# Kernel optimization log

Measured on AMD Instinct MI355X. Metric: run time of the kernel, lower is better.

## Reference

```python
import jax, jax.numpy as jnp
import numpy as np

B, C, N = 8, 128, 32768


def setup_inputs() -> dict:
    key = jax.random.key(0)
    ks = jax.random.split(key, 16)
    def g(k, shape, scale=0.05):
        return jax.random.normal(k, shape, dtype=jnp.float32) * scale
    return {
        "x": jax.random.normal(ks[0], (B, C, N), dtype=jnp.float32),
        "y": jax.random.normal(ks[1], (B, C, N), dtype=jnp.float32),
        "q_w": g(ks[2], (C, C)), "q_b": g(ks[3], (C,)),
        "k_w": g(ks[4], (C, C)), "k_b": g(ks[5], (C,)),
        "v1_w": g(ks[6], (C, C)), "v1_b": g(ks[7], (C,)),
        "v2_w": g(ks[8], (C, C)), "v2_b": g(ks[9], (C,)),
        "t1_w": g(ks[10], (2 * C, 2 * C)), "t1_b": g(ks[11], (2 * C,)),
        "t2_w": g(ks[12], (C, 2 * C)), "t2_b": g(ks[13], (C,)),
    }


def reference(x, y, q_w, q_b, k_w, k_b, v1_w, v1_b, v2_w, v2_b,
              t1_w, t1_b, t2_w, t2_b):
    # num_heads = 1, head_dim = C. Conv1d with kernel 1 == pointwise matmul.
    c = x.shape[1]
    pconv = lambda w, b, z: jnp.einsum('oc,bcn->bon', w, z) + b[None, :, None]
    x_q = pconv(q_w, q_b, y)    # [B,C,N]
    x_k = pconv(k_w, k_b, x)    # [B,C,N]
    x_v = pconv(v1_w, v1_b, x)  # [B,C,N]
    y_v = pconv(v2_w, v2_b, y)  # [B,C,N]
    x_con = jnp.concatenate([x_q, x_k], axis=1)                 # [B,2C,N]
    v_con = jnp.concatenate([y_v.transpose(0, 2, 1),
                             x_v.transpose(0, 2, 1)], axis=2)   # [B,N,2C]
    scale = jnp.sqrt(jnp.float32(2 * c))
    energy = jnp.einsum('bcn,bdn->bcd', x_con, x_con) / scale   # [B,2C,2C]
    e = jax.nn.relu(energy @ t1_w.T + t1_b)                     # [B,2C,2C]
    e = jax.nn.relu(e @ t2_w.T + t2_b)                          # [B,2C,C]
    attn = jax.nn.softmax(e, axis=-1)                           # [B,2C,C]
    x_r = jnp.einsum('bnd,bdc->bnc', v_con, attn)               # [B,N,C]
    return x_r.transpose(0, 2, 1)                               # [B,C,N]
```

## Files before the change

### kernel.cpp

```cpp
#include <hip/hip_runtime.h>

constexpr int CH   = 128;
constexpr int TWOC = 256;
constexpr int NPTS = 32768;
constexpr int NB   = 8;
constexpr int KC   = 2048;

constexpr int KC3    = 1024;
constexpr int KSTAGE = 128;
constexpr int NST    = KC3 / KSTAGE;
constexpr int NCHUNK = NPTS / KC3;

typedef _Float16 half8 __attribute__((ext_vector_type(8)));
typedef float floatx4 __attribute__((ext_vector_type(4)));

constexpr size_t OFF_G  = 0;
constexpr size_t OFF_S  = 524288;
constexpr size_t OFF_P  = 526336;
constexpr size_t OFF_H  = 528384;
constexpr size_t OFF_E  = 1052672;
constexpr size_t OFF_E1 = 1576960;
constexpr size_t OFF_E2 = 2101248;
constexpr size_t OFF_AT = 2363392;
constexpr size_t OFF_C0 = 2625536;
constexpr size_t OFF_MH = 2626560;
constexpr size_t OFF_ZH = 2757632;
constexpr size_t OFF_GP = OFF_ZH + 33554432;
constexpr size_t GP_LEN = (size_t)3 * NB * NCHUNK * 128 * 128;
constexpr size_t WS_NEED_NEW = (OFF_ZH + 33554432) * sizeof(float);
constexpr size_t WS_NEED_V3  = (OFF_GP + GP_LEN) * sizeof(float);


__global__ __launch_bounds__(256) void convert_kernel(
    const float* __restrict__ x, const float* __restrict__ y,
    _Float16* __restrict__ Zh, float* __restrict__ S)
{
  const int seg = blockIdx.x;
  const int r   = blockIdx.y;
  const int b   = blockIdx.z;
  const float* src = ((r < CH) ? (y + ((size_t)b*CH + r)*NPTS)
                               : (x + ((size_t)b*CH + (r-CH))*NPTS)) + (size_t)seg*4096;
  _Float16* dst = Zh + ((size_t)b*TWOC + r)*NPTS + (size_t)seg*4096;
  const int tid = threadIdx.x;

  float s = 0.f;
  const float4* s4 = (const float4*)(src + tid*16);
  union { uint4 u; _Float16 h[8]; } p0, p1;
  float4 a = s4[0], bq = s4[1], c = s4[2], d = s4[3];
  p0.h[0]=(_Float16)a.x;  p0.h[1]=(_Float16)a.y;  p0.h[2]=(_Float16)a.z;  p0.h[3]=(_Float16)a.w;
  p0.h[4]=(_Float16)bq.x; p0.h[5]=(_Float16)bq.y; p0.h[6]=(_Float16)bq.z; p0.h[7]=(_Float16)bq.w;
  p1.h[0]=(_Float16)c.x;  p1.h[1]=(_Float16)c.y;  p1.h[2]=(_Float16)c.z;  p1.h[3]=(_Float16)c.w;
  p1.h[4]=(_Float16)d.x;  p1.h[5]=(_Float16)d.y;  p1.h[6]=(_Float16)d.z;  p1.h[7]=(_Float16)d.w;
  s += a.x+a.y+a.z+a.w + bq.x+bq.y+bq.z+bq.w + c.x+c.y+c.z+c.w + d.x+d.y+d.z+d.w;
  *(uint4*)(dst + tid*16)     = p0.u;
  *(uint4*)(dst + tid*16 + 8) = p1.u;

  for (int off = 32; off > 0; off >>= 1) s += __shfl_down(s, off);
  if ((tid & 63) == 0) atomicAdd(&S[b*TWOC + r], s);
}

__global__ __launch_bounds__(256) void gram_mfma3(
    const _Float16* __restrict__ Zh, float* __restrict__ G, float* __restrict__ GP)
{
  __shared__ __align__(16) _Float16 As[2][128 * KSTAGE];
  __shared__ __align__(16) _Float16 Bs[2][128 * KSTAGE];

  const int hw    = blockIdx.x;
  const int xcd   = hw & 7;
  const int local = hw >> 3;
  const int t     = local % 3;
  const int grp   = local / 3;
  const int gidx  = xcd * 32 + grp;
  const int kc    = gidx & 31;
  const int b     = gidx >> 5;

  const int i0 = (t == 0) ? 0 : CH;
  const int j0 = (t == 2) ? CH : 0;
  const _Float16* Ar = Zh + ((size_t)b*TWOC + i0)*NPTS + (size_t)kc*KC3;
  const _Float16* Br = Zh + ((size_t)b*TWOC + j0)*NPTS + (size_t)kc*KC3;

  const int tid   = threadIdx.x;
  const int lane  = tid & 63;
  const int wave  = tid >> 6;
  const int mbase = (wave & 1) * 64;
  const int nbase = (wave >> 1) * 64;
  const int m0    = lane & 15;
  const int quad  = lane >> 4;

  const int srow = (wave * 512) >> 4;

#define STAGE(buf, k0)                                                        \
  {                                                                           \
    _Pragma("unroll")                                                         \
    for (int i = 0; i < 8; i++) {                                             \
      const int s = wave*512 + i*64 + lane;                                   \
      const int r = s >> 4;                                                   \
      const int g = s & 15;                                                   \
      const int gs = g ^ (r & 7);                                             \
      __builtin_amdgcn_global_load_lds(                                       \
        (const __attribute__((address_space(1))) void*)(Ar + (size_t)r*NPTS + (k0) + gs*8), \
        (__attribute__((address_space(3))) void*)&As[buf][(wave*512 + i*64)*8], \
        16, 0, 0);                                                            \
      __builtin_amdgcn_global_load_lds(                                       \
        (const __attribute__((address_space(1))) void*)(Br + (size_t)r*NPTS + (k0) + gs*8), \
        (__attribute__((address_space(3))) void*)&Bs[buf][(wave*512 + i*64)*8], \
        16, 0, 0);                                                            \
    }                                                                         \
  }

  floatx4 acc[4][4];
  #pragma unroll
  for (int i = 0; i < 4; i++)
    #pragma unroll
    for (int j = 0; j < 4; j++) acc[i][j] = (floatx4){0.f,0.f,0.f,0.f};

  (void)srow;
  STAGE(0, 0);

  int cur = 0;
  for (int st = 0; st < NST; ++st) {
    if (st + 1 < NST) {
      STAGE(cur ^ 1, (st + 1) * KSTAGE);
      asm volatile("s_waitcnt vmcnt(16)" ::: "memory");
    } else {
      asm volatile("s_waitcnt vmcnt(0)" ::: "memory");
    }
    __builtin_amdgcn_s_barrier();

    #pragma unroll
    for (int kk = 0; kk < 4; kk++) {
      half8 af[4], bf[4];
      #pragma unroll
      for (int i = 0; i < 4; i++) {
        const int ra = mbase + i*16 + m0;
        const int ga = (kk*4 + quad) ^ (ra & 7);
        af[i] = *(const half8*)&As[cur][ra*KSTAGE + ga*8];
        const int rb = nbase + i*16 + m0;
        const int gb = (kk*4 + quad) ^ (rb & 7);
        bf[i] = *(const half8*)&Bs[cur][rb*KSTAGE + gb*8];
      }
      #pragma unroll
      for (int i = 0; i < 4; i++)
        #pragma unroll
        for (int j = 0; j < 4; j++)
          acc[i][j] = __builtin_amdgcn_mfma_f32_16x16x32_f16(af[i], bf[j], acc[i][j], 0, 0, 0);
    }

    __builtin_amdgcn_s_barrier();
    cur ^= 1;
  }
#undef STAGE

  if (GP != nullptr) {
    float* gp = GP + (((size_t)(b*3 + t)*NCHUNK + kc) * (128*128));
    #pragma unroll
    for (int i = 0; i < 4; i++)
      #pragma unroll
      for (int j = 0; j < 4; j++)
        #pragma unroll
        for (int rg = 0; rg < 4; rg++) {
          const int row = mbase + i*16 + quad*4 + rg;
          const int col = nbase + j*16 + m0;
          gp[row*128 + col] = acc[i][j][rg];
        }
  } else {
    #pragma unroll
    for (int i = 0; i < 4; i++)
      #pragma unroll
      for (int j = 0; j < 4; j++)
        #pragma unroll
        for (int rg = 0; rg < 4; rg++) {
          const int row = i0 + mbase + i*16 + quad*4 + rg;
          const int col = j0 + nbase + j*16 + m0;
          atomicAdd(&G[((size_t)b*TWOC + row)*TWOC + col], acc[i][j][rg]);
        }
  }
}

__global__ __launch_bounds__(256) void greduce_kernel(
    const float* __restrict__ GP, float* __restrict__ G)
{
  const int t   = blockIdx.y;
  const int b   = blockIdx.z;
  const int idx = blockIdx.x * 256 + threadIdx.x;
  const float* gp = GP + ((size_t)(b*3 + t)*NCHUNK) * (128*128) + idx;
  float s = 0.f;
  #pragma unroll
  for (int k = 0; k < NCHUNK; k++) s += gp[(size_t)k * (128*128)];
  const int i0 = (t == 0) ? 0 : CH;
  const int j0 = (t == 2) ? CH : 0;
  const int row = idx >> 7, col = idx & 127;
  G[((size_t)b*TWOC + i0 + row)*TWOC + j0 + col] = s;
}

__global__ __launch_bounds__(256) void out_mfma(
    const _Float16* __restrict__ Zh, const _Float16* __restrict__ Mh,
    const float* __restrict__ C0, float* __restrict__ out)
{
  const int n0 = blockIdx.x * 128;
  const int b  = blockIdx.y;

  __shared__ __align__(16) _Float16 As[128*64];
  __shared__ __align__(16) _Float16 Bs[128*72];

  const int tid   = threadIdx.x;
  const int lane  = tid & 63;
  const int wave  = tid >> 6;
  const int mbase = (wave & 1) * 64;
  const int nbase = (wave >> 1) * 64;
  const int m0    = lane & 15;
  const int quad  = lane >> 4;

  const int srow  = tid >> 1;
  const int gbase = (tid & 1) * 4;
  const int dl    = tid >> 4;
  const int ng    = tid & 15;

  floatx4 acc[4][4];
  #pragma unroll
  for (int i = 0; i < 4; i++)
    #pragma unroll
    for (int j = 0; j < 4; j++) acc[i][j] = (floatx4){0.f,0.f,0.f,0.f};

  for (int d0 = 0; d0 < TWOC; d0 += 64) {
    __syncthreads();
    #pragma unroll
    for (int q = 0; q < 4; q++) {
      const int g  = gbase + q;
      const int gp = g ^ (srow & 7);
      *(uint4*)&As[(size_t)(srow*8 + gp)*8] =
          *(const uint4*)(Mh + ((size_t)b*CH + srow)*TWOC + d0 + g*8);
    }
    #pragma unroll
    for (int ds = 0; ds < 4; ds++) {
      const int d = dl + ds*16;
      union { uint4 u; _Float16 h[8]; } v;
      v.u = *(const uint4*)(Zh + ((size_t)b*TWOC + d0 + d)*NPTS + n0 + ng*8);
      #pragma unroll
      for (int e = 0; e < 8; e++)
        Bs[(size_t)(ng*8 + e)*72 + d] = v.h[e];
    }
    __syncthreads();
    #pragma unroll
    for (int ks = 0; ks < 2; ks++) {
      half8 af[4], bf[4];
      #pragma unroll
      for (int i = 0; i < 4; i++) {
        const int ra = mbase + i*16 + m0;
        const int ga = (ks*4 + quad) ^ (ra & 7);
        af[i] = *(const half8*)&As[(size_t)(ra*8 + ga)*8];
        const int rn = nbase + i*16 + m0;
        bf[i] = *(const half8*)&Bs[(size_t)rn*72 + ks*32 + quad*8];
      }
      #pragma unroll
      for (int i = 0; i < 4; i++)
        #pragma unroll
        for (int j = 0; j < 4; j++)
          acc[i][j] = __builtin_amdgcn_mfma_f32_16x16x32_f16(af[i], bf[j], acc[i][j], 0, 0, 0);
    }
  }

  #pragma unroll
  for (int i = 0; i < 4; i++) {
    #pragma unroll
    for (int rg = 0; rg < 4; rg++) {
      const int c  = mbase + i*16 + quad*4 + rg;
      const float cv = C0[b*CH + c];
      #pragma unroll
      for (int j = 0; j < 4; j++) {
        const int n = n0 + nbase + j*16 + m0;
        out[((size_t)b*CH + c)*NPTS + n] = acc[i][j][rg] + cv;
      }
    }
  }
}

__global__ void mout_f16_kernel(const float* __restrict__ ATT, const float* __restrict__ v1w,
                                const float* __restrict__ v2w, const float* __restrict__ v1b,
                                const float* __restrict__ v2b, _Float16* __restrict__ Mh,
                                float* __restrict__ C0)
{
  const int c = blockIdx.x, b = blockIdx.y, j = threadIdx.x;
  __shared__ float acol[TWOC];
  acol[j] = ATT[((size_t)b*TWOC + j)*CH + c];
  __syncthreads();
  float acc = 0.f;
  if (j < CH) {
    for (int d = 0; d < CH; d++) acc = fmaf(acol[d], v2w[(size_t)d*CH + j], acc);
  } else {
    const int jj = j - CH;
    for (int d = 0; d < CH; d++) acc = fmaf(acol[CH + d], v1w[(size_t)d*CH + jj], acc);
  }
  Mh[((size_t)b*CH + c)*TWOC + j] = (_Float16)acc;
  if (j == 0) {
    float s = 0.f;
    for (int d = 0; d < CH; d++) s += acol[d]*v2b[d] + acol[CH+d]*v1b[d];
    C0[b*CH + c] = s;
  }
}

__global__ void pmirror_kernel(const float* __restrict__ S, const float* __restrict__ qw,
                               const float* __restrict__ kw, float* __restrict__ P,
                               float* __restrict__ G)
{
  const int b = blockIdx.x;
  const int tid = threadIdx.x;
  const float* w = (tid < CH) ? (qw + (size_t)tid*CH) : (kw + (size_t)(tid-CH)*CH);
  const float* s = S + b*TWOC + ((tid < CH) ? 0 : CH);
  float acc = 0.f;
  for (int j = 0; j < CH; j++) acc = fmaf(w[j], s[j], acc);
  P[b*TWOC + tid] = acc;

  float* Gb = G + (size_t)b * TWOC * TWOC;
  for (int idx = tid; idx < CH*CH; idx += 256) {
    const int i2 = idx >> 7, j2 = idx & 127;
    Gb[(size_t)i2*TWOC + CH + j2] = Gb[(size_t)(CH + j2)*TWOC + i2];
  }
}

__global__ void h_kernel(const float* __restrict__ G, const float* __restrict__ qw,
                         const float* __restrict__ kw, float* __restrict__ H)
{
  const int i = blockIdx.x, b = blockIdx.y, k = threadIdx.x;
  const float* w = (i < CH) ? (qw + (size_t)i*CH) : (kw + (size_t)(i-CH)*CH);
  const int jbase = (i < CH) ? 0 : CH;
  const float* g = G + ((size_t)b*TWOC + jbase)*TWOC + k;
  float acc = 0.f;
  for (int j = 0; j < CH; j++) acc = fmaf(w[j], g[(size_t)j*TWOC], acc);
  H[((size_t)b*TWOC + i)*TWOC + k] = acc;
}

__global__ void e_kernel(const float* __restrict__ H, const float* __restrict__ qw,
                         const float* __restrict__ kw, const float* __restrict__ qb,
                         const float* __restrict__ kb, const float* __restrict__ P,
                         float* __restrict__ E)
{
  const int i = blockIdx.x, b = blockIdx.y, j = threadIdx.x;
  const float* h = H + ((size_t)b*TWOC + i)*TWOC + ((j < CH) ? 0 : CH);
  const float* w = (j < CH) ? (qw + (size_t)j*CH) : (kw + (size_t)(j-CH)*CH);
  const float bcj = (j < CH) ? qb[j] : kb[j-CH];
  const float bci = (i < CH) ? qb[i] : kb[i-CH];
  const float4* h4 = (const float4*)h;
  const float4* w4 = (const float4*)w;
  float acc = 0.f;
  for (int k = 0; k < CH/4; k++) {
    const float4 hv = h4[k], wv = w4[k];
    acc += hv.x*wv.x + hv.y*wv.y + hv.z*wv.z + hv.w*wv.w;
  }
  acc += P[b*TWOC+i]*bcj + bci*P[b*TWOC+j] + (float)NPTS * bci * bcj;
  E[((size_t)b*TWOC + i)*TWOC + j] = acc * (1.0f/16.0f);
}

__global__ void t1_kernel(const float* __restrict__ E, const float* __restrict__ t1w,
                          const float* __restrict__ t1b, float* __restrict__ E1)
{
  const int i = blockIdx.x, b = blockIdx.y, j = threadIdx.x;
  const float4* e4 = (const float4*)(E + ((size_t)b*TWOC + i)*TWOC);
  const float4* w4 = (const float4*)(t1w + (size_t)j*TWOC);
  float acc = t1b[j];
  for (int k = 0; k < TWOC/4; k++) {
    const float4 ev = e4[k], wv = w4[k];
    acc += ev.x*wv.x + ev.y*wv.y + ev.z*wv.z + ev.w*wv.w;
  }
  E1[((size_t)b*TWOC + i)*TWOC + j] = fmaxf(acc, 0.f);
}

__global__ void t2_kernel(const float* __restrict__ E1, const float* __restrict__ t2w,
                          const float* __restrict__ t2b, float* __restrict__ E2)
{
  const int i = blockIdx.x, b = blockIdx.y, j = threadIdx.x;
  const float4* e4 = (const float4*)(E1 + ((size_t)b*TWOC + i)*TWOC);
  const float4* w4 = (const float4*)(t2w + (size_t)j*TWOC);
  float acc = t2b[j];
  for (int k = 0; k < TWOC/4; k++) {
    const float4 ev = e4[k], wv = w4[k];
    acc += ev.x*wv.x + ev.y*wv.y + ev.z*wv.z + ev.w*wv.w;
  }
  E2[((size_t)b*TWOC + i)*CH + j] = fmaxf(acc, 0.f);
}

__global__ void softmax_kernel(const float* __restrict__ E2, float* __restrict__ ATT)
{
  const int b = blockIdx.x;
  const int i = threadIdx.x;
  const float* r = E2  + ((size_t)b*TWOC + i)*CH;
  float*       o = ATT + ((size_t)b*TWOC + i)*CH;
  float m = -1e30f;
  for (int j = 0; j < CH; j++) m = fmaxf(m, r[j]);
  float s = 0.f;
  for (int j = 0; j < CH; j++) s += expf(r[j] - m);
  const float inv = 1.f / s;
  for (int j = 0; j < CH; j++) o[j] = expf(r[j] - m) * inv;
}

__global__ __launch_bounds__(256) void gram_kernel(
    const float* __restrict__ x, const float* __restrict__ y,
    float* __restrict__ G, float* __restrict__ S)
{
  const int t  = blockIdx.x;
  const int kc = blockIdx.y;
  const int b  = blockIdx.z;
  const float* Ab = (t == 0) ? y : x;
  const float* Bb = (t == 2) ? x : y;
  const int growA = (t == 0) ? 0 : CH;
  const int gcolB = (t == 2) ? CH : 0;
  const float* Ap = Ab + (size_t)b * CH * NPTS + (size_t)kc * KC;
  const float* Bp = Bb + (size_t)b * CH * NPTS + (size_t)kc * KC;

  __shared__ __align__(16) float As[8][128];
  __shared__ __align__(16) float Bs[8][128];

  const int tid  = threadIdx.x;
  const int ti   = tid >> 4;
  const int tj   = tid & 15;
  const int lrow = tid >> 1;
  const int lk4  = (tid & 1) * 4;

  const float* arow = Ap + (size_t)lrow * NPTS + lk4;
  const float* brow = Bp + (size_t)lrow * NPTS + lk4;

  float acc[8][8];
  #pragma unroll
  for (int i = 0; i < 8; i++)
    #pragma unroll
    for (int j = 0; j < 8; j++) acc[i][j] = 0.f;
  float asum = 0.f;

  for (int k0 = 0; k0 < KC; k0 += 8) {
    const float4 av = *(const float4*)(arow + k0);
    const float4 bv = *(const float4*)(brow + k0);
    __syncthreads();
    As[lk4+0][lrow] = av.x; As[lk4+1][lrow] = av.y;
    As[lk4+2][lrow] = av.z; As[lk4+3][lrow] = av.w;
    Bs[lk4+0][lrow] = bv.x; Bs[lk4+1][lrow] = bv.y;
    Bs[lk4+2][lrow] = bv.z; Bs[lk4+3][lrow] = bv.w;
    asum += av.x + av.y + av.z + av.w;
    __syncthreads();
    #pragma unroll
    for (int kk = 0; kk < 8; kk++) {
      float a[8], bb[8];
      *(float4*)&a[0]  = *(const float4*)&As[kk][ti*8];
      *(float4*)&a[4]  = *(const float4*)&As[kk][ti*8+4];
      *(float4*)&bb[0] = *(const float4*)&Bs[kk][tj*8];
      *(float4*)&bb[4] = *(const float4*)&Bs[kk][tj*8+4];
      #pragma unroll
      for (int ii = 0; ii < 8; ii++)
        #pragma unroll
        for (int jj = 0; jj < 8; jj++)
          acc[ii][jj] = fmaf(a[ii], bb[jj], acc[ii][jj]);
    }
  }

  float* Gp = G + ((size_t)b * TWOC + growA) * TWOC + gcolB;
  #pragma unroll
  for (int ii = 0; ii < 8; ii++)
    #pragma unroll
    for (int jj = 0; jj < 8; jj++)
      atomicAdd(&Gp[(size_t)(ti*8+ii) * TWOC + (tj*8+jj)], acc[ii][jj]);

  if (t == 0)      atomicAdd(&S[b*TWOC + lrow],      asum);
  else if (t == 2) atomicAdd(&S[b*TWOC + CH + lrow], asum);
}

__global__ void mout_f32_kernel(const float* __restrict__ ATT, const float* __restrict__ v1w,
                                const float* __restrict__ v2w, const float* __restrict__ v1b,
                                const float* __restrict__ v2b, float* __restrict__ M,
                                float* __restrict__ C0)
{
  const int c = blockIdx.x, b = blockIdx.y, j = threadIdx.x;
  __shared__ float acol[TWOC];
  acol[j] = ATT[((size_t)b*TWOC + j)*CH + c];
  __syncthreads();
  float acc = 0.f;
  if (j < CH) {
    for (int d = 0; d < CH; d++) acc = fmaf(acol[d], v2w[(size_t)d*CH + j], acc);
  } else {
    const int jj = j - CH;
    for (int d = 0; d < CH; d++) acc = fmaf(acol[CH + d], v1w[(size_t)d*CH + jj], acc);
  }
  M[((size_t)b*CH + c)*TWOC + j] = acc;
  if (j == 0) {
    float s = 0.f;
    for (int d = 0; d < CH; d++) s += acol[d]*v2b[d] + acol[CH+d]*v1b[d];
    C0[b*CH + c] = s;
  }
}

__global__ __launch_bounds__(256) void out_kernel(
    const float* __restrict__ x, const float* __restrict__ y,
    const float* __restrict__ M, const float* __restrict__ C0,
    float* __restrict__ out)
{
  const int b  = blockIdx.y;
  const int n0 = blockIdx.x * 64;
  const int tid = threadIdx.x;
  const int tc = tid & 15;
  const int tn = tid >> 4;

  __shared__ __align__(16) float Ms[64][128];
  __shared__ __align__(16) float Zs[64][64];

  float acc[8][4];
  #pragma unroll
  for (int i = 0; i < 8; i++)
    #pragma unroll
    for (int j = 0; j < 4; j++) acc[i][j] = 0.f;

  const float* Mb = M + (size_t)b * CH * TWOC;

  for (int chunk = 0; chunk < 4; chunk++) {
    const int kbase = chunk * 64;
    const float* Zsrc = ((chunk < 2) ? y : x) + (size_t)b * CH * NPTS
                        + (size_t)((chunk & 1) * 64) * NPTS;
    __syncthreads();
    {
      const int c   = tid >> 1;
      const int kb2 = (tid & 1) * 32;
      const float* mr = Mb + (size_t)c * TWOC + kbase + kb2;
      #pragma unroll
      for (int q = 0; q < 8; q++) {
        const float4 v = *(const float4*)(mr + q*4);
        Ms[kb2 + q*4 + 0][c] = v.x;
        Ms[kb2 + q*4 + 1][c] = v.y;
        Ms[kb2 + q*4 + 2][c] = v.z;
        Ms[kb2 + q*4 + 3][c] = v.w;
      }
      const int kk  = tid >> 2;
      const int nb4 = (tid & 3) * 4;
      const float* zr = Zsrc + (size_t)kk * NPTS + n0 + nb4;
      #pragma unroll
      for (int q = 0; q < 4; q++)
        *(float4*)&Zs[kk][nb4 + q*16] = *(const float4*)(zr + q*16);
    }
    __syncthreads();
    #pragma unroll 8
    for (int kk = 0; kk < 64; kk++) {
      float a[8], zz[4];
      *(float4*)&a[0]  = *(const float4*)&Ms[kk][tc*8];
      *(float4*)&a[4]  = *(const float4*)&Ms[kk][tc*8+4];
      *(float4*)&zz[0] = *(const float4*)&Zs[kk][tn*4];
      #pragma unroll
      for (int ii = 0; ii < 8; ii++)
        #pragma unroll
        for (int jj = 0; jj < 4; jj++)
          acc[ii][jj] = fmaf(a[ii], zz[jj], acc[ii][jj]);
    }
  }

  #pragma unroll
  for (int ii = 0; ii < 8; ii++) {
    const int c = tc*8 + ii;
    const float cv = C0[b*CH + c];
    float4 o;
    o.x = acc[ii][0] + cv; o.y = acc[ii][1] + cv;
    o.z = acc[ii][2] + cv; o.w = acc[ii][3] + cv;
    *(float4*)&out[((size_t)b*CH + c)*NPTS + n0 + tn*4] = o;
  }
}

extern "C" void kernel_launch(void* const* d_in, const int* in_sizes, int n_in,
                              void* d_out, int out_size, void* d_ws, size_t ws_size,
                              hipStream_t stream)
{
  const float* x   = (const float*)d_in[0];
  const float* y   = (const float*)d_in[1];
  const float* qw  = (const float*)d_in[2];
  const float* qb  = (const float*)d_in[3];
  const float* kw  = (const float*)d_in[4];
  const float* kb  = (const float*)d_in[5];
  const float* v1w = (const float*)d_in[6];
  const float* v1b = (const float*)d_in[7];
  const float* v2w = (const float*)d_in[8];
  const float* v2b = (const float*)d_in[9];
  const float* t1w = (const float*)d_in[10];
  const float* t1b = (const float*)d_in[11];
  const float* t2w = (const float*)d_in[12];
  const float* t2b = (const float*)d_in[13];

  float* ws = (float*)d_ws;
  float* G  = ws + OFF_G;
  float* S  = ws + OFF_S;
  float* P  = ws + OFF_P;
  float* H  = ws + OFF_H;
  float* E  = ws + OFF_E;
  float* E1 = ws + OFF_E1;
  float* E2 = ws + OFF_E2;
  float* AT = ws + OFF_AT;
  float* C0 = ws + OFF_C0;
  float* outp = (float*)d_out;

  hipMemsetAsync(d_ws, 0, (OFF_S + 2048) * sizeof(float), stream);

  if (ws_size >= WS_NEED_NEW) {
    _Float16* Mh = (_Float16*)(ws + OFF_MH);
    _Float16* Zh = (_Float16*)(ws + OFF_ZH);
    const bool useGP = (ws_size >= WS_NEED_V3);
    float* GP = useGP ? (ws + OFF_GP) : nullptr;

    convert_kernel<<<dim3(NPTS/4096, TWOC, NB), 256, 0, stream>>>(x, y, Zh, S);
    gram_mfma3    <<<dim3(3 * NCHUNK * NB),     256, 0, stream>>>(Zh, G, GP);
    if (useGP)
      greduce_kernel<<<dim3(64, 3, NB),         256, 0, stream>>>(GP, G);
    pmirror_kernel<<<dim3(NB),                  256, 0, stream>>>(S, qw, kw, P, G);
    h_kernel      <<<dim3(TWOC, NB),            256, 0, stream>>>(G, qw, kw, H);
    e_kernel      <<<dim3(TWOC, NB),            256, 0, stream>>>(H, qw, kw, qb, kb, P, E);
    t1_kernel     <<<dim3(TWOC, NB),            256, 0, stream>>>(E, t1w, t1b, E1);
    t2_kernel     <<<dim3(TWOC, NB),            128, 0, stream>>>(E1, t2w, t2b, E2);
    softmax_kernel<<<dim3(NB),                  256, 0, stream>>>(E2, AT);
    mout_f16_kernel<<<dim3(CH, NB),             256, 0, stream>>>(AT, v1w, v2w, v1b, v2b, Mh, C0);
    out_mfma      <<<dim3(NPTS/128, NB),        256, 0, stream>>>(Zh, Mh, C0, outp);
  } else {
    float* Mo = ws + OFF_MH;
    gram_kernel   <<<dim3(3, NPTS/KC, NB), 256, 0, stream>>>(x, y, G, S);
    pmirror_kernel<<<dim3(NB),             256, 0, stream>>>(S, qw, kw, P, G);
    h_kernel      <<<dim3(TWOC, NB),       256, 0, stream>>>(G, qw, kw, H);
    e_kernel      <<<dim3(TWOC, NB),       256, 0, stream>>>(H, qw, kw, qb, kb, P, E);
    t1_kernel     <<<dim3(TWOC, NB),       256, 0, stream>>>(E, t1w, t1b, E1);
    t2_kernel     <<<dim3(TWOC, NB),       128, 0, stream>>>(E1, t2w, t2b, E2);
    softmax_kernel<<<dim3(NB),             256, 0, stream>>>(E2, AT);
    mout_f32_kernel<<<dim3(CH, NB),        256, 0, stream>>>(AT, v1w, v2w, v1b, v2b, Mo, C0);
    out_kernel    <<<dim3(NPTS/64, NB),    256, 0, stream>>>(x, y, Mo, C0, outp);
  }
}
```

Measured before the change: 699.1 us.

## Fuse attention-head small kernels into one per-row kernel and swizzle out_mfma LDS

Replaces the chain of h, e, t1, t2, softmax kernels (and pmirror on the main path) with a single per-row kernel that keeps intermediates in shared memory and computes the bias projection inline. The greduce kernel now writes the mirrored Gram block directly. The convert kernel switches to coalesced strided float4 loads, and out_mfma's B tile in LDS gets an XOR swizzle to reduce bank conflicts. This removes several launches and global round trips in exchange for redundant per-block recomputation of P.

```diff
diff --git a/kernel.cpp b/kernel.cpp
--- a/kernel.cpp
+++ b/kernel.cpp
@@ -44,16 +44,15 @@
   const int tid = threadIdx.x;
 
   float s = 0.f;
-  const float4* s4 = (const float4*)(src + tid*16);
-  union { uint4 u; _Float16 h[8]; } p0, p1;
-  float4 a = s4[0], bq = s4[1], c = s4[2], d = s4[3];
-  p0.h[0]=(_Float16)a.x;  p0.h[1]=(_Float16)a.y;  p0.h[2]=(_Float16)a.z;  p0.h[3]=(_Float16)a.w;
-  p0.h[4]=(_Float16)bq.x; p0.h[5]=(_Float16)bq.y; p0.h[6]=(_Float16)bq.z; p0.h[7]=(_Float16)bq.w;
-  p1.h[0]=(_Float16)c.x;  p1.h[1]=(_Float16)c.y;  p1.h[2]=(_Float16)c.z;  p1.h[3]=(_Float16)c.w;
-  p1.h[4]=(_Float16)d.x;  p1.h[5]=(_Float16)d.y;  p1.h[6]=(_Float16)d.z;  p1.h[7]=(_Float16)d.w;
-  s += a.x+a.y+a.z+a.w + bq.x+bq.y+bq.z+bq.w + c.x+c.y+c.z+c.w + d.x+d.y+d.z+d.w;
-  *(uint4*)(dst + tid*16)     = p0.u;
-  *(uint4*)(dst + tid*16 + 8) = p1.u;
+  #pragma unroll
+  for (int it = 0; it < 4; it++) {
+    const int idx = it*1024 + tid*4;
+    const float4 v = *(const float4*)(src + idx);
+    union { uint2 u; _Float16 h[4]; } p;
+    p.h[0]=(_Float16)v.x; p.h[1]=(_Float16)v.y; p.h[2]=(_Float16)v.z; p.h[3]=(_Float16)v.w;
+    *(uint2*)(dst + idx) = p.u;
+    s += v.x + v.y + v.z + v.w;
+  }
 
   for (int off = 32; off > 0; off >>= 1) s += __shfl_down(s, off);
   if ((tid & 63) == 0) atomicAdd(&S[b*TWOC + r], s);
@@ -86,8 +85,6 @@
   const int nbase = (wave >> 1) * 64;
   const int m0    = lane & 15;
   const int quad  = lane >> 4;
-
-  const int srow = (wave * 512) >> 4;
 
 #define STAGE(buf, k0)                                                        \
   {                                                                           \
@@ -114,7 +111,6 @@
     #pragma unroll
     for (int j = 0; j < 4; j++) acc[i][j] = (floatx4){0.f,0.f,0.f,0.f};
 
-  (void)srow;
   STAGE(0, 0);
 
   int cur = 0;
@@ -191,6 +187,105 @@
   const int j0 = (t == 2) ? CH : 0;
   const int row = idx >> 7, col = idx & 127;
   G[((size_t)b*TWOC + i0 + row)*TWOC + j0 + col] = s;
+  if (t == 1)
+    G[((size_t)b*TWOC + col)*TWOC + CH + row] = s;
+}
+
+__global__ __launch_bounds__(256) void att_row_kernel(
+    const float* __restrict__ G, const float* __restrict__ S,
+    const float* __restrict__ qw, const float* __restrict__ kw,
+    const float* __restrict__ qb, const float* __restrict__ kb,
+    const float* __restrict__ t1w, const float* __restrict__ t1b,
+    const float* __restrict__ t2w, const float* __restrict__ t2b,
+    float* __restrict__ ATT)
+{
+  const int i   = blockIdx.x;
+  const int b   = blockIdx.y;
+  const int tid = threadIdx.x;
+
+  __shared__ float Hs[TWOC];
+  __shared__ float Es[TWOC];
+  __shared__ float E1s[TWOC];
+  __shared__ float Ss[TWOC];
+  __shared__ float red[8];
+
+  Ss[tid] = S[b*TWOC + tid];
+
+  const int jbase = (i < CH) ? 0 : CH;
+  const float* wi  = (i < CH) ? (qw + (size_t)i*CH) : (kw + (size_t)(i-CH)*CH);
+  const float bci  = (i < CH) ? qb[i] : kb[i-CH];
+
+  float hacc = 0.f;
+  const float* gcol = G + ((size_t)b*TWOC + jbase)*TWOC + tid;
+  for (int j2 = 0; j2 < CH; j2++) hacc = fmaf(wi[j2], gcol[(size_t)j2*TWOC], hacc);
+  Hs[tid] = hacc;
+  __syncthreads();
+
+  {
+    const int j = tid;
+    const float* wj = (j < CH) ? (qw + (size_t)j*CH) : (kw + (size_t)(j-CH)*CH);
+    const float bcj = (j < CH) ? qb[j] : kb[j-CH];
+    const float* hseg = Hs + ((j < CH) ? 0 : CH);
+    const float* ssj  = Ss + ((j < CH) ? 0 : CH);
+    const float* ssi  = Ss + ((i < CH) ? 0 : CH);
+    const float4* w4  = (const float4*)wj;
+    const float4* wi4 = (const float4*)wi;
+    float eacc = 0.f, pj = 0.f, pi = 0.f;
+    for (int k = 0; k < CH/4; k++) {
+      const float4 wv  = w4[k];
+      const float4 hv  = *(const float4*)&hseg[k*4];
+      const float4 sv  = *(const float4*)&ssj[k*4];
+      const float4 wiv = wi4[k];
+      const float4 siv = *(const float4*)&ssi[k*4];
+      eacc += hv.x*wv.x + hv.y*wv.y + hv.z*wv.z + hv.w*wv.w;
+      pj   += sv.x*wv.x + sv.y*wv.y + sv.z*wv.z + sv.w*wv.w;
+      pi   += siv.x*wiv.x + siv.y*wiv.y + siv.z*wiv.z + siv.w*wiv.w;
+    }
+    eacc += pi*bcj + bci*pj + (float)NPTS * bci * bcj;
+    Es[j] = eacc * (1.0f/16.0f);
+  }
+  __syncthreads();
+
+  {
+    float a1 = t1b[tid];
+    const float4* wr = (const float4*)(t1w + (size_t)tid*TWOC);
+    for (int k = 0; k < TWOC/4; k++) {
+      const float4 wv = wr[k];
+      const float4 ev = *(const float4*)&Es[k*4];
+      a1 += ev.x*wv.x + ev.y*wv.y + ev.z*wv.z + ev.w*wv.w;
+    }
+    E1s[tid] = fmaxf(a1, 0.f);
+  }
+  __syncthreads();
+
+  float e2 = 0.f;
+  if (tid < CH) {
+    float a2 = t2b[tid];
+    const float4* wr = (const float4*)(t2w + (size_t)tid*TWOC);
+    for (int k = 0; k < TWOC/4; k++) {
+      const float4 wv = wr[k];
+      const float4 ev = *(const float4*)&E1s[k*4];
+      a2 += ev.x*wv.x + ev.y*wv.y + ev.z*wv.z + ev.w*wv.w;
+    }
+    e2 = fmaxf(a2, 0.f);
+  }
+
+  const int lane = tid & 63, wv_ = tid >> 6;
+  float m = (tid < CH) ? e2 : -1e30f;
+  for (int off = 32; off > 0; off >>= 1) m = fmaxf(m, __shfl_xor(m, off));
+  if (lane == 0) red[wv_] = m;
+  __syncthreads();
+  m = fmaxf(red[0], red[1]);
+
+  float ex = (tid < CH) ? expf(e2 - m) : 0.f;
+  float sum = ex;
+  for (int off = 32; off > 0; off >>= 1) sum += __shfl_xor(sum, off);
+  if (lane == 0) red[4 + wv_] = sum;
+  __syncthreads();
+  sum = red[4] + red[5];
+
+  if (tid < CH)
+    ATT[((size_t)b*TWOC + i)*CH + tid] = ex / sum;
 }
 
 __global__ __launch_bounds__(256) void out_mfma(
@@ -233,12 +328,17 @@
     }
     #pragma unroll
     for (int ds = 0; ds < 4; ds++) {
-      const int d = dl + ds*16;
+      const int d    = dl + ds*16;
+      const int gd   = d >> 3;
+      const int dlow = d & 7;
       union { uint4 u; _Float16 h[8]; } v;
       v.u = *(const uint4*)(Zh + ((size_t)b*TWOC + d0 + d)*NPTS + n0 + ng*8);
       #pragma unroll
-      for (int e = 0; e < 8; e++)
-        Bs[(size_t)(ng*8 + e)*72 + d] = v.h[e];
+      for (int e = 0; e < 8; e++) {
+        const int n  = ng*8 + e;
+        const int pg = gd ^ (ng & 7);
+        Bs[(size_t)n*72 + pg*8 + dlow] = v.h[e];
+      }
     }
     __syncthreads();
     #pragma unroll
@@ -249,8 +349,10 @@
         const int ra = mbase + i*16 + m0;
         const int ga = (ks*4 + quad) ^ (ra & 7);
         af[i] = *(const half8*)&As[(size_t)(ra*8 + ga)*8];
-        const int rn = nbase + i*16 + m0;
-        bf[i] = *(const half8*)&Bs[(size_t)rn*72 + ks*32 + quad*8];
+        const int rn  = nbase + i*16 + m0;
+        const int g   = ks*4 + quad;
+        const int pgr = g ^ ((rn >> 3) & 7);
+        bf[i] = *(const half8*)&Bs[(size_t)rn*72 + pgr*8];
       }
       #pragma unroll
       for (int i = 0; i < 4; i++)
@@ -305,92 +407,11 @@
 {
   const int b = blockIdx.x;
   const int tid = threadIdx.x;
-  const float* w = (tid < CH) ? (qw + (size_t)tid*CH) : (kw + (size_t)(tid-CH)*CH);
-  const float* s = S + b*TWOC + ((tid < CH) ? 0 : CH);
-  float acc = 0.f;
-  for (int j = 0; j < CH; j++) acc = fmaf(w[j], s[j], acc);
-  P[b*TWOC + tid] = acc;
-
   float* Gb = G + (size_t)b * TWOC * TWOC;
   for (int idx = tid; idx < CH*CH; idx += 256) {
     const int i2 = idx >> 7, j2 = idx & 127;
     Gb[(size_t)i2*TWOC + CH + j2] = Gb[(size_t)(CH + j2)*TWOC + i2];
   }
-}
-
-__global__ void h_kernel(const float* __restrict__ G, const float* __restrict__ qw,
-                         const float* __restrict__ kw, float* __restrict__ H)
-{
-  const int i = blockIdx.x, b = blockIdx.y, k = threadIdx.x;
-  const float* w = (i < CH) ? (qw + (size_t)i*CH) : (kw + (size_t)(i-CH)*CH);
-  const int jbase = (i < CH) ? 0 : CH;
-  const float* g = G + ((size_t)b*TWOC + jbase)*TWOC + k;
-  float acc = 0.f;
-  for (int j = 0; j < CH; j++) acc = fmaf(w[j], g[(size_t)j*TWOC], acc);
-  H[((size_t)b*TWOC + i)*TWOC + k] = acc;
-}
-
-__global__ void e_kernel(const float* __restrict__ H, const float* __restrict__ qw,
-                         const float* __restrict__ kw, const float* __restrict__ qb,
-                         const float* __restrict__ kb, const float* __restrict__ P,
-                         float* __restrict__ E)
-{
-  const int i = blockIdx.x, b = blockIdx.y, j = threadIdx.x;
-  const float* h = H + ((size_t)b*TWOC + i)*TWOC + ((j < CH) ? 0 : CH);
-  const float* w = (j < CH) ? (qw + (size_t)j*CH) : (kw + (size_t)(j-CH)*CH);
-  const float bcj = (j < CH) ? qb[j] : kb[j-CH];
-  const float bci = (i < CH) ? qb[i] : kb[i-CH];
-  const float4* h4 = (const float4*)h;
-  const float4* w4 = (const float4*)w;
-  float acc = 0.f;
-  for (int k = 0; k < CH/4; k++) {
-    const float4 hv = h4[k], wv = w4[k];
-    acc += hv.x*wv.x + hv.y*wv.y + hv.z*wv.z + hv.w*wv.w;
-  }
-  acc += P[b*TWOC+i]*bcj + bci*P[b*TWOC+j] + (float)NPTS * bci * bcj;
-  E[((size_t)b*TWOC + i)*TWOC + j] = acc * (1.0f/16.0f);
-}
-
-__global__ void t1_kernel(const float* __restrict__ E, const float* __restrict__ t1w,
-                          const float* __restrict__ t1b, float* __restrict__ E1)
-{
-  const int i = blockIdx.x, b = blockIdx.y, j = threadIdx.x;
-  const float4* e4 = (const float4*)(E + ((size_t)b*TWOC + i)*TWOC);
-  const float4* w4 = (const float4*)(t1w + (size_t)j*TWOC);
-  float acc = t1b[j];
-  for (int k = 0; k < TWOC/4; k++) {
-    const float4 ev = e4[k], wv = w4[k];
-    acc += ev.x*wv.x + ev.y*wv.y + ev.z*wv.z + ev.w*wv.w;
-  }
-  E1[((size_t)b*TWOC + i)*TWOC + j] = fmaxf(acc, 0.f);
-}
-
-__global__ void t2_kernel(const float* __restrict__ E1, const float* __restrict__ t2w,
-                          const float* __restrict__ t2b, float* __restrict__ E2)
-{
-  const int i = blockIdx.x, b = blockIdx.y, j = threadIdx.x;
-  const float4* e4 = (const float4*)(E1 + ((size_t)b*TWOC + i)*TWOC);
-  const float4* w4 = (const float4*)(t2w + (size_t)j*TWOC);
-  float acc = t2b[j];
-  for (int k = 0; k < TWOC/4; k++) {
-    const float4 ev = e4[k], wv = w4[k];
-    acc += ev.x*wv.x + ev.y*wv.y + ev.z*wv.z + ev.w*wv.w;
-  }
-  E2[((size_t)b*TWOC + i)*CH + j] = fmaxf(acc, 0.f);
-}
-
-__global__ void softmax_kernel(const float* __restrict__ E2, float* __restrict__ ATT)
-{
-  const int b = blockIdx.x;
-  const int i = threadIdx.x;
-  const float* r = E2  + ((size_t)b*TWOC + i)*CH;
-  float*       o = ATT + ((size_t)b*TWOC + i)*CH;
-  float m = -1e30f;
-  for (int j = 0; j < CH; j++) m = fmaxf(m, r[j]);
-  float s = 0.f;
-  for (int j = 0; j < CH; j++) s += expf(r[j] - m);
-  const float inv = 1.f / s;
-  for (int j = 0; j < CH; j++) o[j] = expf(r[j] - m) * inv;
 }
 
 __global__ __launch_bounds__(256) void gram_kernel(
@@ -581,10 +602,6 @@
   float* G  = ws + OFF_G;
   float* S  = ws + OFF_S;
   float* P  = ws + OFF_P;
-  float* H  = ws + OFF_H;
-  float* E  = ws + OFF_E;
-  float* E1 = ws + OFF_E1;
-  float* E2 = ws + OFF_E2;
   float* AT = ws + OFF_AT;
   float* C0 = ws + OFF_C0;
   float* outp = (float*)d_out;
@@ -601,23 +618,18 @@
     gram_mfma3    <<<dim3(3 * NCHUNK * NB),     256, 0, stream>>>(Zh, G, GP);
     if (useGP)
       greduce_kernel<<<dim3(64, 3, NB),         256, 0, stream>>>(GP, G);
-    pmirror_kernel<<<dim3(NB),                  256, 0, stream>>>(S, qw, kw, P, G);
-    h_kernel      <<<dim3(TWOC, NB),            256, 0, stream>>>(G, qw, kw, H);
-    e_kernel      <<<dim3(TWOC, NB),            256, 0, stream>>>(H, qw, kw, qb, kb, P, E);
-    t1_kernel     <<<dim3(TWOC, NB),            256, 0, stream>>>(E, t1w, t1b, E1);
-    t2_kernel     <<<dim3(TWOC, NB),            128, 0, stream>>>(E1, t2w, t2b, E2);
-    softmax_kernel<<<dim3(NB),                  256, 0, stream>>>(E2, AT);
+    else
+      pmirror_kernel<<<dim3(NB),                256, 0, stream>>>(S, qw, kw, P, G);
+    att_row_kernel<<<dim3(TWOC, NB),            256, 0, stream>>>(G, S, qw, kw, qb, kb,
+                                                                  t1w, t1b, t2w, t2b, AT);
     mout_f16_kernel<<<dim3(CH, NB),             256, 0, stream>>>(AT, v1w, v2w, v1b, v2b, Mh, C0);
     out_mfma      <<<dim3(NPTS/128, NB),        256, 0, stream>>>(Zh, Mh, C0, outp);
   } else {
     float* Mo = ws + OFF_MH;
     gram_kernel   <<<dim3(3, NPTS/KC, NB), 256, 0, stream>>>(x, y, G, S);
     pmirror_kernel<<<dim3(NB),             256, 0, stream>>>(S, qw, kw, P, G);
-    h_kernel      <<<dim3(TWOC, NB),       256, 0, stream>>>(G, qw, kw, H);
-    e_kernel      <<<dim3(TWOC, NB),       256, 0, stream>>>(H, qw, kw, qb, kb, P, E);
-    t1_kernel     <<<dim3(TWOC, NB),       256, 0, stream>>>(E, t1w, t1b, E1);
-    t2_kernel     <<<dim3(TWOC, NB),       128, 0, stream>>>(E1, t2w, t2b, E2);
-    softmax_kernel<<<dim3(NB),             256, 0, stream>>>(E2, AT);
+    att_row_kernel<<<dim3(TWOC, NB),       256, 0, stream>>>(G, S, qw, kw, qb, kb,
+                                                             t1w, t1b, t2w, t2b, AT);
     mout_f32_kernel<<<dim3(CH, NB),        256, 0, stream>>>(AT, v1w, v2w, v1b, v2b, Mo, C0);
     out_kernel    <<<dim3(NPTS/64, NB),    256, 0, stream>>>(x, y, Mo, C0, outp);
   }
```

Measured after the change: 615.5 us. -12.0%, faster.
